# Kernel tuning notes

Measured on AMD Instinct MI355X. Metric: run time of the kernel, lower is better.

## Reference

```python
import jax, jax.numpy as jnp
import numpy as np

B, SQ, ST, SI = 8, 4096, 77, 16
C, DC, H = 1280, 2048, 20
DH = C // H  # 64
SCALE = 1.0 / np.sqrt(DH).astype(np.float32)
SCALE_ID = 1.0
SCALE_HAIR = 1.0


def setup_inputs() -> dict:
    key = jax.random.key(0)
    ks = jax.random.split(key, 12)
    std = 0.02
    return {
        "hidden_states": jax.random.normal(ks[0], (B, SQ, C), jnp.float32),
        "text_states": jax.random.normal(ks[1], (B, ST, DC), jnp.float32),
        "id_states": jax.random.normal(ks[2], (B, SI, DC), jnp.float32),
        "hair_states": jax.random.normal(ks[3], (B, SI, DC), jnp.float32),
        # weights stored as [in, out] (transpose of torch nn.Linear layout)
        "Wq": jax.random.normal(ks[4], (C, C), jnp.float32) * std,
        "Wk": jax.random.normal(ks[5], (DC, C), jnp.float32) * std,
        "Wv": jax.random.normal(ks[6], (DC, C), jnp.float32) * std,
        "Wo": jax.random.normal(ks[7], (C, C), jnp.float32) * std,
        "b_o": jnp.zeros((C,), jnp.float32),
        "Wk_id": jax.random.normal(ks[8], (DC, C), jnp.float32) * std,
        "Wv_id": jax.random.normal(ks[9], (DC, C), jnp.float32) * std,
        "Wk_hair": jax.random.normal(ks[10], (DC, C), jnp.float32) * std,
        "Wv_hair": jax.random.normal(ks[11], (DC, C), jnp.float32) * std,
    }


def _heads(x):
    # [B, S, C] -> [B, H, S, DH]
    b, s, _ = x.shape
    return x.reshape(b, s, H, DH).transpose(0, 2, 1, 3)


def _merge(x):
    # [B, H, S, DH] -> [B, S, C]
    b, h, s, d = x.shape
    return x.transpose(0, 2, 1, 3).reshape(b, s, h * d)


def _attend(q, k, v):
    # q: [B,H,Sq,DH], k/v: [B,H,Sk,DH]; fp32 scores (attn_fp32=True)
    scores = jnp.einsum("bhqd,bhkd->bhqk", q.astype(jnp.float32), k.astype(jnp.float32)) * SCALE
    p = jax.nn.softmax(scores, axis=-1)
    return jnp.einsum("bhqk,bhkd->bhqd", p, v.astype(jnp.float32))


def reference(hidden_states, text_states, id_states, hair_states, Wq, Wk, Wv, Wo, b_o, Wk_id, Wv_id, Wk_hair, Wv_hair):
    q = _heads(hidden_states @ Wq)
    # base cross-attention to text (standard diffusers AttnProcessor)
    base = _attend(q, _heads(text_states @ Wk), _heads(text_states @ Wv))
    result = _merge(base) @ Wo + b_o
    # ID branch: own K/V projections, shared query and to_out
    out_id = _attend(q, _heads(id_states @ Wk_id), _heads(id_states @ Wv_id))
    result = result + SCALE_ID * (_merge(out_id) @ Wo + b_o)
    # hair branch
    out_h = _attend(q, _heads(hair_states @ Wk_hair), _heads(hair_states @ Wv_hair))
    result = result + SCALE_HAIR * (_merge(out_h) @ Wo + b_o)
    return result
```

## Files before the change

### kernel.cpp

```cpp
#include <hip/hip_runtime.h>
#include <cstdint>
#include <cstddef>

typedef unsigned short u16;
typedef __attribute__((ext_vector_type(4))) float     f32x4_t;
typedef __attribute__((ext_vector_type(8))) __bf16    bf16x8_t;
typedef __attribute__((ext_vector_type(8))) u16       u16x8_t;
typedef __attribute__((ext_vector_type(4))) u16       u16x4_t;
typedef __attribute__((ext_vector_type(4))) float     fvec4_t;

#define DEVI __device__ __forceinline__

constexpr int Bn  = 8;
constexpr int SQn = 4096;
constexpr int STn = 77;
constexpr int SIn = 16;
constexpr int Cn  = 1280;
constexpr int DCn = 2048;
constexpr int Hn  = 20;
constexpr float SCALEf = 0.125f;
constexpr float L2E    = 1.4426950408889634f;

typedef const __attribute__((address_space(1))) void* gas_t;
typedef __attribute__((address_space(3))) void*       las_t;

DEVI u16 f2bf(float f) {
  union { float f; unsigned u; } cv; cv.f = f;
  unsigned u = cv.u;
  return (u16)((u + 0x7FFFu + ((u >> 16) & 1u)) >> 16);
}

__global__ __launch_bounds__(256) void cast_bf16_kernel(
    const float* __restrict__ src, u16* __restrict__ dst, int n8) {
  int i = blockIdx.x * 256 + threadIdx.x;
  if (i >= n8) return;
  const fvec4_t* s4 = (const fvec4_t*)src;
  fvec4_t a = s4[2 * i], b = s4[2 * i + 1];
  u16x8_t o;
  o[0] = f2bf(a[0]); o[1] = f2bf(a[1]); o[2] = f2bf(a[2]); o[3] = f2bf(a[3]);
  o[4] = f2bf(b[0]); o[5] = f2bf(b[1]); o[6] = f2bf(b[2]); o[7] = f2bf(b[3]);
  ((u16x8_t*)dst)[i] = o;
}

struct TrArgs {
  const float* src[8];
  u16*         dst[8];
  int          Kd[8];
};

__global__ __launch_bounds__(256) void transpose_cast_kernel(TrArgs ta) {
  int z = blockIdx.z;
  int K = ta.Kd[z];
  int k0 = blockIdx.x * 32;
  if (k0 >= K) return;
  int n0 = blockIdx.y * 32;
  __shared__ float tile[32][33];
  int tx = threadIdx.x & 31, ty = threadIdx.x >> 5;
  const float* src = ta.src[z];
#pragma unroll
  for (int i = 0; i < 4; i++) {
    int r = ty + 8 * i;
    tile[r][tx] = src[(size_t)(k0 + r) * Cn + n0 + tx];
  }
  __syncthreads();
  u16* dst = ta.dst[z];
#pragma unroll
  for (int i = 0; i < 4; i++) {
    int r = ty + 8 * i;
    dst[(size_t)(n0 + r) * K + k0 + tx] = f2bf(tile[tx][r]);
  }
}

template <int OUT_MODE, int A_HM>
__global__ __launch_bounds__(512, 2) void gemm256_kernel(
    const u16* __restrict__ A, const u16* __restrict__ Bt,
    void* __restrict__ Cout, const float* __restrict__ bias, int M, int K) {
  __shared__ __align__(16) u16 lds[(OUT_MODE == 2) ? 73728 : 65536];
  const int t = threadIdx.x;
  const int w = t >> 6, l = t & 63;
  const int wr = w >> 2, wc = w & 3;
  const int lr = l & 15;
  const int m0 = blockIdx.x * 256, n0 = blockIdx.y * 256;
  const int NT = K >> 6;

  auto bufp = [&](int cb, int op) -> u16* { return lds + (size_t)(cb * 2 + op) * 16384; };

  f32x4_t acc[8][4];
#pragma unroll
  for (int am = 0; am < 8; am++)
#pragma unroll
    for (int an = 0; an < 4; an++) {
      f32x4_t z = {0.f, 0.f, 0.f, 0.f};
      acc[am][an] = z;
    }

  auto stageAll = [&](int cb, int kt) {
    const int k0 = kt * 64;
#pragma unroll
    for (int i = 0; i < 4; i++) {
      int row = i * 64 + w * 8 + (l >> 3);
      int col16 = (l & 7) ^ (row & 7);
      const u16* ga;
      if (A_HM) {
        int gr = m0 + row, bb = gr >> 12, ss = gr & 4095;
        ga = A + (((size_t)bb * Hn + kt) * SQn + ss) * 64 + col16 * 8;
      } else {
        ga = A + (size_t)(m0 + row) * K + k0 + col16 * 8;
      }
      __builtin_amdgcn_global_load_lds((gas_t)ga, (las_t)(bufp(cb, 0) + (size_t)(i * 512 + w * 64) * 8), 16, 0, 0);
      const u16* gb = Bt + (size_t)(n0 + row) * K + k0 + col16 * 8;
      __builtin_amdgcn_global_load_lds((gas_t)gb, (las_t)(bufp(cb, 1) + (size_t)(i * 512 + w * 64) * 8), 16, 0, 0);
    }
  };
  auto readA8 = [&](bf16x8_t (&dst)[8], const u16* bA, int kh) {
#pragma unroll
    for (int m = 0; m < 8; m++) {
      int row = wr * 128 + m * 16 + lr;
      int slot = kh * 4 + (l >> 4);
      dst[m] = *(const bf16x8_t*)&bA[row * 64 + ((slot ^ (row & 7)) * 8)];
    }
  };
  auto readB4 = [&](bf16x8_t (&dst)[4], const u16* bB, int kh) {
#pragma unroll
    for (int n = 0; n < 4; n++) {
      int row = wc * 64 + n * 16 + lr;
      int slot = kh * 4 + (l >> 4);
      dst[n] = *(const bf16x8_t*)&bB[row * 64 + ((slot ^ (row & 7)) * 8)];
    }
  };
  auto mfma32 = [&](bf16x8_t (&Af)[8], bf16x8_t (&Bf)[4]) {
    __builtin_amdgcn_s_setprio(1);
#pragma unroll
    for (int m = 0; m < 8; m++)
#pragma unroll
      for (int n = 0; n < 4; n++)
        acc[m][n] = __builtin_amdgcn_mfma_f32_16x16x32_bf16(Af[m], Bf[n], acc[m][n], 0, 0, 0);
    __builtin_amdgcn_s_setprio(0);
  };

  stageAll(0, 0);
  stageAll(1, 1);
  asm volatile("s_waitcnt vmcnt(8)" ::: "memory");
  __builtin_amdgcn_sched_barrier(0);
  __builtin_amdgcn_s_barrier();

  bf16x8_t Af0[8], Bf0[4], Af1[8], Bf1[4];
  readA8(Af0, bufp(0, 0), 0);
  readB4(Bf0, bufp(0, 1), 0);
  asm volatile("s_waitcnt lgkmcnt(0)" ::: "memory");
  __builtin_amdgcn_sched_barrier(0);

  for (int kt = 0; kt < NT; kt++) {
    const int cb = kt & 1;
    const bool st = (kt + 2 < NT);

    readA8(Af1, bufp(cb, 0), 1);
    readB4(Bf1, bufp(cb, 1), 1);
    __builtin_amdgcn_sched_barrier(0);
    __builtin_amdgcn_s_barrier();
    if (st) stageAll(cb, kt + 2);
    mfma32(Af0, Bf0);
    asm volatile("s_waitcnt lgkmcnt(0)" ::: "memory");
    __builtin_amdgcn_sched_barrier(0);

    if (st) {
      asm volatile("s_waitcnt vmcnt(8)" ::: "memory");
    } else if (kt + 1 < NT) {
      asm volatile("s_waitcnt vmcnt(0)" ::: "memory");
    }
    __builtin_amdgcn_sched_barrier(0);
    __builtin_amdgcn_s_barrier();

    if (kt + 1 < NT) {
      readA8(Af0, bufp(cb ^ 1, 0), 0);
      readB4(Bf0, bufp(cb ^ 1, 1), 0);
      __builtin_amdgcn_sched_barrier(0);
    }
    mfma32(Af1, Bf1);
    asm volatile("s_waitcnt lgkmcnt(0)" ::: "memory");
    __builtin_amdgcn_sched_barrier(0);
  }

  if (OUT_MODE == 1) {
#pragma unroll
    for (int am = 0; am < 8; am++) {
      int rbase = m0 + wr * 128 + am * 16 + (l >> 4) * 4;
#pragma unroll
      for (int an = 0; an < 4; an++) {
        int col = n0 + wc * 64 + an * 16 + lr;
#pragma unroll
        for (int j = 0; j < 4; j++) {
          int r = rbase + j;
          ((float*)Cout)[(size_t)r * Cn + col] = acc[am][an][j] + 3.0f * bias[col];
        }
      }
    }
  } else {
    __syncthreads();
    u16* R = lds + (size_t)w * 9216;
#pragma unroll
    for (int am = 0; am < 8; am++)
#pragma unroll
      for (int an = 0; an < 4; an++)
#pragma unroll
        for (int j = 0; j < 4; j++) {
          int row = am * 16 + (l >> 4) * 4 + j;
          int g = an * 2 + (lr >> 3);
          int gp = g ^ (row & 7);
          R[row * 72 + gp * 8 + (lr & 7)] = f2bf(acc[am][an][j]);
        }
    const int hh = (n0 >> 6) + wc;
    const int rbase = m0 + wr * 128;
    const int bb = rbase >> 12;
    const int ssb = rbase & 4095;
    u16* dstW = (u16*)Cout + (((size_t)bb * Hn + hh) * SQn + ssb) * 64;
#pragma unroll
    for (int it = 0; it < 16; it++) {
      int rr = it * 8 + (l >> 3);
      int gr = l & 7;
      int gp = gr ^ (rr & 7);
      u16x8_t v = *(const u16x8_t*)&R[rr * 72 + gp * 8];
      *(u16x8_t*)&dstW[(size_t)rr * 64 + gr * 8] = v;
    }
  }
}

DEVI void gemm_body(const u16* __restrict__ A, const u16* __restrict__ Bt,
                    u16* __restrict__ Cout, int M, int S, int K, int mtile, int ntile) {
  __shared__ __align__(16) u16 lA[128 * 64];
  __shared__ __align__(16) u16 lB[128 * 64];
  const int t = threadIdx.x;
  const int w = t >> 6, l = t & 63;
  const int wr = w >> 1, wc = w & 1;
  const int m0 = mtile * 128, n0 = ntile * 128;
  const int lr = l & 15, lk = (l >> 4) * 8;

  f32x4_t acc[4][4];
#pragma unroll
  for (int m = 0; m < 4; m++)
#pragma unroll
    for (int n = 0; n < 4; n++) {
      f32x4_t z = {0.f, 0.f, 0.f, 0.f};
      acc[m][n] = z;
    }

  for (int k0 = 0; k0 < K; k0 += 64) {
    __syncthreads();
#pragma unroll
    for (int i = 0; i < 4; i++) {
      int c = i * 256 + t;
      int row = c >> 3, ch = c & 7;
      int rA = m0 + row;
      rA = rA < M ? rA : M - 1;
      const u16* ga = A + (size_t)rA * K + k0 + ch * 8;
      __builtin_amdgcn_global_load_lds((gas_t)ga, (las_t)&lA[(i * 256 + w * 64) * 8], 16, 0, 0);
      const u16* gb = Bt + (size_t)(n0 + row) * K + k0 + ch * 8;
      __builtin_amdgcn_global_load_lds((gas_t)gb, (las_t)&lB[(i * 256 + w * 64) * 8], 16, 0, 0);
    }
    __syncthreads();
#pragma unroll
    for (int kk = 0; kk < 2; kk++) {
      bf16x8_t af[4], bf[4];
#pragma unroll
      for (int m = 0; m < 4; m++)
        af[m] = *(const bf16x8_t*)&lA[(64 * wr + 16 * m + lr) * 64 + kk * 32 + lk];
#pragma unroll
      for (int n = 0; n < 4; n++)
        bf[n] = *(const bf16x8_t*)&lB[(64 * wc + 16 * n + lr) * 64 + kk * 32 + lk];
#pragma unroll
      for (int m = 0; m < 4; m++)
#pragma unroll
        for (int n = 0; n < 4; n++)
          acc[m][n] = __builtin_amdgcn_mfma_f32_16x16x32_bf16(af[m], bf[n], acc[m][n], 0, 0, 0);
    }
  }

  const int rj = (l >> 4) * 4;
  const int hh = ntile * 2 + wc;
#pragma unroll
  for (int m = 0; m < 4; m++) {
    int rbase = m0 + 64 * wr + 16 * m + rj;
#pragma unroll
    for (int n = 0; n < 4; n++) {
      int dd = 16 * n + lr;
#pragma unroll
      for (int j = 0; j < 4; j++) {
        int r = rbase + j;
        if (r < M) {
          int bb = r / S, ss = r - bb * S;
          Cout[(((size_t)bb * Hn + hh) * S + ss) * 64 + dd] = f2bf(acc[m][n][j]);
        }
      }
    }
  }
}

struct KV6 {
  const u16* A[6];
  const u16* Bt[6];
  u16*       Cp[6];
  int        M[6];
  int        S[6];
};

__global__ __launch_bounds__(256) void gemm_kv_kernel(KV6 kv) {
  int z = blockIdx.z;
  int M = kv.M[z];
  if ((int)blockIdx.x * 128 >= M) return;
  gemm_body(kv.A[z], kv.Bt[z], kv.Cp[z], M, kv.S[z], DCn, blockIdx.x, blockIdx.y);
}

__global__ __launch_bounds__(256) void attn_kernel(
    const u16* __restrict__ q,
    const u16* __restrict__ ktx, const u16* __restrict__ vtx,
    const u16* __restrict__ kid, const u16* __restrict__ vid,
    const u16* __restrict__ kh,  const u16* __restrict__ vh,
    u16* __restrict__ osum) {
  __shared__ __align__(16) u16 KP[4 * 16 * 136];
  __shared__ __align__(16) u16 Vt[64 * 128];

  const int t = threadIdx.x, w = t >> 6, l = t & 63;
  const int bh = blockIdx.y;
  const int lr = l & 15, lk = (l >> 4) * 8;

  const u16* qB   = q   + ((size_t)bh) * SQn * 64;
  const u16* ktxB = ktx + ((size_t)bh) * STn * 64;
  const u16* vtxB = vtx + ((size_t)bh) * STn * 64;
  const u16* kidB = kid + ((size_t)bh) * SIn * 64;
  const u16* vidB = vid + ((size_t)bh) * SIn * 64;
  const u16* khB  = kh  + ((size_t)bh) * SIn * 64;
  const u16* vhB  = vh  + ((size_t)bh) * SIn * 64;
  u16*       oB   = osum + ((size_t)bh) * SQn * 64;

  for (int i = t; i < 112 * 8; i += 256) {
    int row = i >> 3, ch = i & 7;
    u16x8_t vv;
#pragma unroll
    for (int x = 0; x < 8; x++) vv[x] = 0;
    if (row < 77)
      vv = *(const u16x8_t*)(ktxB + (size_t)row * 64 + ch * 8);
    else if (row >= 80 && row < 96)
      vv = *(const u16x8_t*)(kidB + (size_t)(row - 80) * 64 + ch * 8);
    else if (row >= 96)
      vv = *(const u16x8_t*)(khB + (size_t)(row - 96) * 64 + ch * 8);
    *(u16x8_t*)&KP[row * 72 + ch * 8] = vv;
  }
  for (int i = t; i < 128 * 8; i += 256) {
    int key = i >> 3, ch = i & 7;
    u16x8_t vv;
#pragma unroll
    for (int x = 0; x < 8; x++) vv[x] = 0;
    if (key < 77)
      vv = *(const u16x8_t*)(vtxB + (size_t)key * 64 + ch * 8);
    else if (key >= 80 && key < 96)
      vv = *(const u16x8_t*)(vidB + (size_t)(key - 80) * 64 + ch * 8);
    else if (key >= 96 && key < 112)
      vv = *(const u16x8_t*)(vhB + (size_t)(key - 96) * 64 + ch * 8);
    int G = key >> 3, wk = key & 7;
#pragma unroll
    for (int x = 0; x < 8; x++) {
      int d = ch * 8 + x;
      int Gs = G ^ x ^ ch;
      Vt[d * 128 + Gs * 8 + wk] = vv[x];
    }
  }
  __syncthreads();

  bf16x8_t kf[7][2];
#pragma unroll
  for (int tt = 0; tt < 7; tt++)
#pragma unroll
    for (int kk = 0; kk < 2; kk++)
      kf[tt][kk] = *(const bf16x8_t*)&KP[(tt * 16 + lr) * 72 + kk * 32 + lk];
  __syncthreads();

  u16* Pw = &KP[w * 16 * 136];
  {
    u16x4_t z4; z4[0] = 0; z4[1] = 0; z4[2] = 0; z4[3] = 0;
    *(u16x4_t*)&Pw[(l >> 2) * 136 + 112 + (l & 3) * 4] = z4;
  }

  for (int rt = 0; rt < 4; rt++) {
    const int s0 = blockIdx.x * 256 + w * 64 + rt * 16;
    bf16x8_t qf[2];
#pragma unroll
    for (int kk = 0; kk < 2; kk++)
      qf[kk] = *(const bf16x8_t*)&qB[(size_t)(s0 + lr) * 64 + kk * 32 + lk];

    f32x4_t sc[7];
#pragma unroll
    for (int tt = 0; tt < 7; tt++) {
      f32x4_t z = {0.f, 0.f, 0.f, 0.f};
      z = __builtin_amdgcn_mfma_f32_16x16x32_bf16(qf[0], kf[tt][0], z, 0, 0, 0);
      z = __builtin_amdgcn_mfma_f32_16x16x32_bf16(qf[1], kf[tt][1], z, 0, 0, 0);
      sc[tt] = z;
    }
#pragma unroll
    for (int tt = 0; tt < 7; tt++)
#pragma unroll
      for (int j = 0; j < 4; j++) sc[tt][j] *= SCALEf;
    if (lr >= 13) {
#pragma unroll
      for (int j = 0; j < 4; j++) sc[4][j] = -3.0e38f;
    }

    float mx[4], sm[4], inv[4];

#pragma unroll
    for (int j = 0; j < 4; j++) {
      float m = sc[0][j];
      m = fmaxf(m, sc[1][j]); m = fmaxf(m, sc[2][j]);
      m = fmaxf(m, sc[3][j]); m = fmaxf(m, sc[4][j]);
      mx[j] = m;
    }
#pragma unroll
    for (int d = 1; d < 16; d <<= 1)
#pragma unroll
      for (int j = 0; j < 4; j++) mx[j] = fmaxf(mx[j], __shfl_xor(mx[j], d));
#pragma unroll
    for (int j = 0; j < 4; j++) sm[j] = 0.f;
#pragma unroll
    for (int tt = 0; tt < 5; tt++)
#pragma unroll
      for (int j = 0; j < 4; j++) {
        float p = __builtin_amdgcn_exp2f((sc[tt][j] - mx[j]) * L2E);
        sc[tt][j] = p;
        sm[j] += p;
      }
#pragma unroll
    for (int d = 1; d < 16; d <<= 1)
#pragma unroll
      for (int j = 0; j < 4; j++) sm[j] += __shfl_xor(sm[j], d);
#pragma unroll
    for (int j = 0; j < 4; j++) inv[j] = __builtin_amdgcn_rcpf(sm[j]);
#pragma unroll
    for (int tt = 0; tt < 5; tt++)
#pragma unroll
      for (int j = 0; j < 4; j++) {
        __bf16 pb = (__bf16)(sc[tt][j] * inv[j]);
        Pw[((l >> 4) * 4 + j) * 136 + tt * 16 + lr] = *(u16*)&pb;
      }

#pragma unroll
    for (int j = 0; j < 4; j++) mx[j] = sc[5][j];
#pragma unroll
    for (int d = 1; d < 16; d <<= 1)
#pragma unroll
      for (int j = 0; j < 4; j++) mx[j] = fmaxf(mx[j], __shfl_xor(mx[j], d));
#pragma unroll
    for (int j = 0; j < 4; j++) {
      float p = __builtin_amdgcn_exp2f((sc[5][j] - mx[j]) * L2E);
      sc[5][j] = p;
      sm[j] = p;
    }
#pragma unroll
    for (int d = 1; d < 16; d <<= 1)
#pragma unroll
      for (int j = 0; j < 4; j++) sm[j] += __shfl_xor(sm[j], d);
#pragma unroll
    for (int j = 0; j < 4; j++) {
      __bf16 pb = (__bf16)(sc[5][j] * __builtin_amdgcn_rcpf(sm[j]));
      Pw[((l >> 4) * 4 + j) * 136 + 80 + lr] = *(u16*)&pb;
    }

#pragma unroll
    for (int j = 0; j < 4; j++) mx[j] = sc[6][j];
#pragma unroll
    for (int d = 1; d < 16; d <<= 1)
#pragma unroll
      for (int j = 0; j < 4; j++) mx[j] = fmaxf(mx[j], __shfl_xor(mx[j], d));
#pragma unroll
    for (int j = 0; j < 4; j++) {
      float p = __builtin_amdgcn_exp2f((sc[6][j] - mx[j]) * L2E);
      sc[6][j] = p;
      sm[j] = p;
    }
#pragma unroll
    for (int d = 1; d < 16; d <<= 1)
#pragma unroll
      for (int j = 0; j < 4; j++) sm[j] += __shfl_xor(sm[j], d);
#pragma unroll
    for (int j = 0; j < 4; j++) {
      __bf16 pb = (__bf16)(sc[6][j] * __builtin_amdgcn_rcpf(sm[j]));
      Pw[((l >> 4) * 4 + j) * 136 + 96 + lr] = *(u16*)&pb;
    }

    f32x4_t oacc[4];
#pragma unroll
    for (int n = 0; n < 4; n++) {
      f32x4_t z = {0.f, 0.f, 0.f, 0.f};
      oacc[n] = z;
    }
#pragma unroll
    for (int ktile = 0; ktile < 4; ktile++) {
      bf16x8_t pf = *(const bf16x8_t*)&Pw[lr * 136 + ktile * 32 + lk];
#pragma unroll
      for (int n = 0; n < 4; n++) {
        int d = 16 * n + lr;
        int Gs = (4 * ktile + (l >> 4)) ^ (d & 7) ^ ((d >> 3) & 7);
        bf16x8_t vf = *(const bf16x8_t*)&Vt[d * 128 + Gs * 8];
        oacc[n] = __builtin_amdgcn_mfma_f32_16x16x32_bf16(pf, vf, oacc[n], 0, 0, 0);
      }
    }
#pragma unroll
    for (int n = 0; n < 4; n++)
#pragma unroll
      for (int j = 0; j < 4; j++) {
        int srow = s0 + (l >> 4) * 4 + j;
        __bf16 ob = (__bf16)oacc[n][j];
        oB[(size_t)srow * 64 + 16 * n + lr] = *(u16*)&ob;
      }
  }
}

extern "C" void kernel_launch(void* const* d_in, const int* in_sizes, int n_in,
                              void* d_out, int out_size, void* d_ws, size_t ws_size,
                              hipStream_t stream) {
  (void)in_sizes; (void)n_in; (void)out_size; (void)ws_size;
  const float* hidden  = (const float*)d_in[0];
  const float* text    = (const float*)d_in[1];
  const float* ids     = (const float*)d_in[2];
  const float* hair    = (const float*)d_in[3];
  const float* Wq      = (const float*)d_in[4];
  const float* Wk      = (const float*)d_in[5];
  const float* Wv      = (const float*)d_in[6];
  const float* Wo      = (const float*)d_in[7];
  const float* b_o     = (const float*)d_in[8];
  const float* Wk_id   = (const float*)d_in[9];
  const float* Wv_id   = (const float*)d_in[10];
  const float* Wk_hair = (const float*)d_in[11];
  const float* Wv_hair = (const float*)d_in[12];
  float* out = (float*)d_out;

  char* ws = (char*)d_ws;
  size_t off = 0;
  auto carve = [&](size_t bytes) -> char* {
    char* p = ws + off;
    off += (bytes + 255) & ~(size_t)255;
    return p;
  };

  u16* h_bf    = (u16*)carve((size_t)Bn * SQn * Cn * 2);
  u16* q_bf    = (u16*)carve((size_t)Bn * SQn * Cn * 2);
  u16* text_bf = (u16*)carve((size_t)Bn * STn * DCn * 2);
  u16* id_bf   = (u16*)carve((size_t)Bn * SIn * DCn * 2);
  u16* hair_bf = (u16*)carve((size_t)Bn * SIn * DCn * 2);
  u16* Wq_t    = (u16*)carve((size_t)Cn * Cn * 2);
  u16* Wo_t    = (u16*)carve((size_t)Cn * Cn * 2);
  u16* Wk_t    = (u16*)carve((size_t)DCn * Cn * 2);
  u16* Wv_t    = (u16*)carve((size_t)DCn * Cn * 2);
  u16* Wkid_t  = (u16*)carve((size_t)DCn * Cn * 2);
  u16* Wvid_t  = (u16*)carve((size_t)DCn * Cn * 2);
  u16* Wkh_t   = (u16*)carve((size_t)DCn * Cn * 2);
  u16* Wvh_t   = (u16*)carve((size_t)DCn * Cn * 2);
  u16* k_text  = (u16*)carve((size_t)Bn * STn * Cn * 2);
  u16* v_text  = (u16*)carve((size_t)Bn * STn * Cn * 2);
  u16* k_id    = (u16*)carve((size_t)Bn * SIn * Cn * 2);
  u16* v_id    = (u16*)carve((size_t)Bn * SIn * Cn * 2);
  u16* k_hr    = (u16*)carve((size_t)Bn * SIn * Cn * 2);
  u16* v_hr    = (u16*)carve((size_t)Bn * SIn * Cn * 2);
  u16* attn_sum = h_bf;

  {
    int n8 = Bn * SQn * Cn / 8;
    cast_bf16_kernel<<<dim3((n8 + 255) / 256), 256, 0, stream>>>(hidden, h_bf, n8);
  }
  {
    int n8 = Bn * STn * DCn / 8;
    cast_bf16_kernel<<<dim3((n8 + 255) / 256), 256, 0, stream>>>(text, text_bf, n8);
  }
  {
    int n8 = Bn * SIn * DCn / 8;
    cast_bf16_kernel<<<dim3((n8 + 255) / 256), 256, 0, stream>>>(ids, id_bf, n8);
    cast_bf16_kernel<<<dim3((n8 + 255) / 256), 256, 0, stream>>>(hair, hair_bf, n8);
  }

  {
    TrArgs ta;
    ta.src[0] = Wq;      ta.dst[0] = Wq_t;   ta.Kd[0] = Cn;
    ta.src[1] = Wo;      ta.dst[1] = Wo_t;   ta.Kd[1] = Cn;
    ta.src[2] = Wk;      ta.dst[2] = Wk_t;   ta.Kd[2] = DCn;
    ta.src[3] = Wv;      ta.dst[3] = Wv_t;   ta.Kd[3] = DCn;
    ta.src[4] = Wk_id;   ta.dst[4] = Wkid_t; ta.Kd[4] = DCn;
    ta.src[5] = Wv_id;   ta.dst[5] = Wvid_t; ta.Kd[5] = DCn;
    ta.src[6] = Wk_hair; ta.dst[6] = Wkh_t;  ta.Kd[6] = DCn;
    ta.src[7] = Wv_hair; ta.dst[7] = Wvh_t;  ta.Kd[7] = DCn;
    transpose_cast_kernel<<<dim3(DCn / 32, Cn / 32, 8), 256, 0, stream>>>(ta);
  }

  gemm256_kernel<2, 0><<<dim3(Bn * SQn / 256, Cn / 256), 512, 0, stream>>>(
      h_bf, Wq_t, q_bf, nullptr, Bn * SQn, Cn);

  {
    KV6 kv;
    kv.A[0] = text_bf; kv.Bt[0] = Wk_t;   kv.Cp[0] = k_text; kv.M[0] = Bn * STn; kv.S[0] = STn;
    kv.A[1] = text_bf; kv.Bt[1] = Wv_t;   kv.Cp[1] = v_text; kv.M[1] = Bn * STn; kv.S[1] = STn;
    kv.A[2] = id_bf;   kv.Bt[2] = Wkid_t; kv.Cp[2] = k_id;   kv.M[2] = Bn * SIn; kv.S[2] = SIn;
    kv.A[3] = id_bf;   kv.Bt[3] = Wvid_t; kv.Cp[3] = v_id;   kv.M[3] = Bn * SIn; kv.S[3] = SIn;
    kv.A[4] = hair_bf; kv.Bt[4] = Wkh_t;  kv.Cp[4] = k_hr;   kv.M[4] = Bn * SIn; kv.S[4] = SIn;
    kv.A[5] = hair_bf; kv.Bt[5] = Wvh_t;  kv.Cp[5] = v_hr;   kv.M[5] = Bn * SIn; kv.S[5] = SIn;
    gemm_kv_kernel<<<dim3((Bn * STn + 127) / 128, Cn / 128, 6), 256, 0, stream>>>(kv);
  }

  attn_kernel<<<dim3(SQn / 256, Bn * Hn), 256, 0, stream>>>(
      q_bf, k_text, v_text, k_id, v_id, k_hr, v_hr, attn_sum);

  gemm256_kernel<1, 1><<<dim3(Bn * SQn / 256, Cn / 256), 512, 0, stream>>>(
      attn_sum, Wo_t, out, b_o, Bn * SQn, Cn);
}
```

Measured before the change: 480.8 us.

## Fuse fp32-to-bf16 cast of hidden states into the Q projection GEMM

Removes the standalone cast kernel for hidden_states and has a new Q GEMM kernel load fp32 A tiles into registers, convert to bf16, and write them swizzled into LDS, while B still uses direct global-to-LDS loads. This avoids writing and re-reading a 32768x1280 bf16 intermediate. The trade-off is that the GEMM now reads twice as many A bytes, each A tile is read by 5 column blocks, and the pipeline adds register staging and conversion work that could slow the main loop. The generic GEMM template is reduced to the fp32-output path.

```diff
diff --git a/kernel.cpp b/kernel.cpp
--- a/kernel.cpp
+++ b/kernel.cpp
@@ -71,11 +71,160 @@
   }
 }
 
+__global__ __launch_bounds__(512, 2) void gemm_q_fused_kernel(
+    const float* __restrict__ Af, const u16* __restrict__ Bt,
+    u16* __restrict__ Cout, int M, int K) {
+  __shared__ __align__(16) u16 lds[73728];
+  const int t = threadIdx.x;
+  const int w = t >> 6, l = t & 63;
+  const int wr = w >> 2, wc = w & 3;
+  const int lr = l & 15;
+  const int m0 = blockIdx.x * 256, n0 = blockIdx.y * 256;
+  const int NT = K >> 6;
+
+  auto bufp = [&](int cb, int op) -> u16* { return lds + (size_t)(cb * 2 + op) * 16384; };
+
+  f32x4_t acc[8][4];
+#pragma unroll
+  for (int am = 0; am < 8; am++)
+#pragma unroll
+    for (int an = 0; an < 4; an++) {
+      f32x4_t z = {0.f, 0.f, 0.f, 0.f};
+      acc[am][an] = z;
+    }
+
+  f32x4_t areg[8];
+  auto issueA = [&](int kt) {
+    const int k0 = kt * 64;
+#pragma unroll
+    for (int i = 0; i < 4; i++) {
+      int row = i * 64 + w * 8 + (l >> 3);
+      const float* ga = Af + (size_t)(m0 + row) * K + k0 + (l & 7) * 8;
+      areg[2 * i]     = *(const fvec4_t*)ga;
+      areg[2 * i + 1] = *(const fvec4_t*)(ga + 4);
+    }
+  };
+  auto writeA = [&](int cb) {
+#pragma unroll
+    for (int i = 0; i < 4; i++) {
+      int row = i * 64 + w * 8 + (l >> 3);
+      int gp = (l & 7) ^ (row & 7);
+      u16x8_t o;
+      o[0] = f2bf(areg[2 * i][0]);     o[1] = f2bf(areg[2 * i][1]);
+      o[2] = f2bf(areg[2 * i][2]);     o[3] = f2bf(areg[2 * i][3]);
+      o[4] = f2bf(areg[2 * i + 1][0]); o[5] = f2bf(areg[2 * i + 1][1]);
+      o[6] = f2bf(areg[2 * i + 1][2]); o[7] = f2bf(areg[2 * i + 1][3]);
+      *(u16x8_t*)&bufp(cb, 0)[row * 64 + gp * 8] = o;
+    }
+  };
+  auto issueB = [&](int cb, int kt) {
+    const int k0 = kt * 64;
+#pragma unroll
+    for (int i = 0; i < 4; i++) {
+      int row = i * 64 + w * 8 + (l >> 3);
+      int col16 = (l & 7) ^ (row & 7);
+      const u16* gb = Bt + (size_t)(n0 + row) * K + k0 + col16 * 8;
+      __builtin_amdgcn_global_load_lds((gas_t)gb, (las_t)(bufp(cb, 1) + (size_t)(i * 512 + w * 64) * 8), 16, 0, 0);
+    }
+  };
+  auto readA8 = [&](bf16x8_t (&dst)[8], const u16* bA, int kh) {
+#pragma unroll
+    for (int m = 0; m < 8; m++) {
+      int row = wr * 128 + m * 16 + lr;
+      int slot = kh * 4 + (l >> 4);
+      dst[m] = *(const bf16x8_t*)&bA[row * 64 + ((slot ^ (row & 7)) * 8)];
+    }
+  };
+  auto readB4 = [&](bf16x8_t (&dst)[4], const u16* bB, int kh) {
+#pragma unroll
+    for (int n = 0; n < 4; n++) {
+      int row = wc * 64 + n * 16 + lr;
+      int slot = kh * 4 + (l >> 4);
+      dst[n] = *(const bf16x8_t*)&bB[row * 64 + ((slot ^ (row & 7)) * 8)];
+    }
+  };
+  auto mfma32 = [&](bf16x8_t (&Afr)[8], bf16x8_t (&Bfr)[4]) {
+    __builtin_amdgcn_s_setprio(1);
+#pragma unroll
+    for (int m = 0; m < 8; m++)
+#pragma unroll
+      for (int n = 0; n < 4; n++)
+        acc[m][n] = __builtin_amdgcn_mfma_f32_16x16x32_bf16(Afr[m], Bfr[n], acc[m][n], 0, 0, 0);
+    __builtin_amdgcn_s_setprio(0);
+  };
+
+  issueA(0);
+  writeA(0);
+  issueA(1);
+  issueB(0, 0);
+  issueB(1, 1);
+  asm volatile("s_waitcnt vmcnt(4)" ::: "memory");
+  __builtin_amdgcn_sched_barrier(0);
+  writeA(1);
+  issueA(2);
+  asm volatile("s_waitcnt lgkmcnt(0)" ::: "memory");
+  __builtin_amdgcn_sched_barrier(0);
+  __builtin_amdgcn_s_barrier();
+
+  for (int kt = 0; kt < NT; kt++) {
+    const int cb = kt & 1;
+    const u16* bA = bufp(cb, 0);
+    const u16* bB = bufp(cb, 1);
+    bf16x8_t Afr[8], Bfr[4];
+
+    readA8(Afr, bA, 0);
+    readB4(Bfr, bB, 0);
+    asm volatile("s_waitcnt lgkmcnt(0)" ::: "memory");
+    __builtin_amdgcn_sched_barrier(0);
+    mfma32(Afr, Bfr);
+
+    readA8(Afr, bA, 1);
+    readB4(Bfr, bB, 1);
+    __builtin_amdgcn_s_barrier();
+    asm volatile("s_waitcnt vmcnt(0)" ::: "memory");
+    __builtin_amdgcn_sched_barrier(0);
+    if (kt + 2 < NT) writeA(cb);
+    if (kt + 3 < NT) issueA(kt + 3);
+    if (kt + 2 < NT) issueB(cb, kt + 2);
+    asm volatile("s_waitcnt lgkmcnt(0)" ::: "memory");
+    __builtin_amdgcn_sched_barrier(0);
+    mfma32(Afr, Bfr);
+    __builtin_amdgcn_s_barrier();
+  }
+
+  __syncthreads();
+  u16* R = lds + (size_t)w * 9216;
+#pragma unroll
+  for (int am = 0; am < 8; am++)
+#pragma unroll
+    for (int an = 0; an < 4; an++)
+#pragma unroll
+      for (int j = 0; j < 4; j++) {
+        int row = am * 16 + (l >> 4) * 4 + j;
+        int g = an * 2 + (lr >> 3);
+        int gp = g ^ (row & 7);
+        R[row * 72 + gp * 8 + (lr & 7)] = f2bf(acc[am][an][j]);
+      }
+  const int hh = (n0 >> 6) + wc;
+  const int rbase = m0 + wr * 128;
+  const int bb = rbase >> 12;
+  const int ssb = rbase & 4095;
+  u16* dstW = Cout + (((size_t)bb * Hn + hh) * SQn + ssb) * 64;
+#pragma unroll
+  for (int it = 0; it < 16; it++) {
+    int rr = it * 8 + (l >> 3);
+    int gr = l & 7;
+    int gp = gr ^ (rr & 7);
+    u16x8_t v = *(const u16x8_t*)&R[rr * 72 + gp * 8];
+    *(u16x8_t*)&dstW[(size_t)rr * 64 + gr * 8] = v;
+  }
+}
+
 template <int OUT_MODE, int A_HM>
 __global__ __launch_bounds__(512, 2) void gemm256_kernel(
     const u16* __restrict__ A, const u16* __restrict__ Bt,
     void* __restrict__ Cout, const float* __restrict__ bias, int M, int K) {
-  __shared__ __align__(16) u16 lds[(OUT_MODE == 2) ? 73728 : 65536];
+  __shared__ __align__(16) u16 lds[65536];
   const int t = threadIdx.x;
   const int w = t >> 6, l = t & 63;
   const int wr = w >> 2, wc = w & 3;
@@ -181,46 +330,17 @@
     __builtin_amdgcn_sched_barrier(0);
   }
 
-  if (OUT_MODE == 1) {
-#pragma unroll
-    for (int am = 0; am < 8; am++) {
-      int rbase = m0 + wr * 128 + am * 16 + (l >> 4) * 4;
-#pragma unroll
-      for (int an = 0; an < 4; an++) {
-        int col = n0 + wc * 64 + an * 16 + lr;
-#pragma unroll
-        for (int j = 0; j < 4; j++) {
-          int r = rbase + j;
-          ((float*)Cout)[(size_t)r * Cn + col] = acc[am][an][j] + 3.0f * bias[col];
-        }
+#pragma unroll
+  for (int am = 0; am < 8; am++) {
+    int rbase = m0 + wr * 128 + am * 16 + (l >> 4) * 4;
+#pragma unroll
+    for (int an = 0; an < 4; an++) {
+      int col = n0 + wc * 64 + an * 16 + lr;
+#pragma unroll
+      for (int j = 0; j < 4; j++) {
+        int r = rbase + j;
+        ((float*)Cout)[(size_t)r * Cn + col] = acc[am][an][j] + 3.0f * bias[col];
       }
-    }
-  } else {
-    __syncthreads();
-    u16* R = lds + (size_t)w * 9216;
-#pragma unroll
-    for (int am = 0; am < 8; am++)
-#pragma unroll
-      for (int an = 0; an < 4; an++)
-#pragma unroll
-        for (int j = 0; j < 4; j++) {
-          int row = am * 16 + (l >> 4) * 4 + j;
-          int g = an * 2 + (lr >> 3);
-          int gp = g ^ (row & 7);
-          R[row * 72 + gp * 8 + (lr & 7)] = f2bf(acc[am][an][j]);
-        }
-    const int hh = (n0 >> 6) + wc;
-    const int rbase = m0 + wr * 128;
-    const int bb = rbase >> 12;
-    const int ssb = rbase & 4095;
-    u16* dstW = (u16*)Cout + (((size_t)bb * Hn + hh) * SQn + ssb) * 64;
-#pragma unroll
-    for (int it = 0; it < 16; it++) {
-      int rr = it * 8 + (l >> 3);
-      int gr = l & 7;
-      int gp = gr ^ (rr & 7);
-      u16x8_t v = *(const u16x8_t*)&R[rr * 72 + gp * 8];
-      *(u16x8_t*)&dstW[(size_t)rr * 64 + gr * 8] = v;
     }
   }
 }
@@ -540,7 +660,7 @@
     return p;
   };
 
-  u16* h_bf    = (u16*)carve((size_t)Bn * SQn * Cn * 2);
+  u16* attn_sum = (u16*)carve((size_t)Bn * SQn * Cn * 2);
   u16* q_bf    = (u16*)carve((size_t)Bn * SQn * Cn * 2);
   u16* text_bf = (u16*)carve((size_t)Bn * STn * DCn * 2);
   u16* id_bf   = (u16*)carve((size_t)Bn * SIn * DCn * 2);
@@ -559,12 +679,7 @@
   u16* v_id    = (u16*)carve((size_t)Bn * SIn * Cn * 2);
   u16* k_hr    = (u16*)carve((size_t)Bn * SIn * Cn * 2);
   u16* v_hr    = (u16*)carve((size_t)Bn * SIn * Cn * 2);
-  u16* attn_sum = h_bf;
-
-  {
-    int n8 = Bn * SQn * Cn / 8;
-    cast_bf16_kernel<<<dim3((n8 + 255) / 256), 256, 0, stream>>>(hidden, h_bf, n8);
-  }
+
   {
     int n8 = Bn * STn * DCn / 8;
     cast_bf16_kernel<<<dim3((n8 + 255) / 256), 256, 0, stream>>>(text, text_bf, n8);
@@ -588,8 +703,8 @@
     transpose_cast_kernel<<<dim3(DCn / 32, Cn / 32, 8), 256, 0, stream>>>(ta);
   }
 
-  gemm256_kernel<2, 0><<<dim3(Bn * SQn / 256, Cn / 256), 512, 0, stream>>>(
-      h_bf, Wq_t, q_bf, nullptr, Bn * SQn, Cn);
+  gemm_q_fused_kernel<<<dim3(Bn * SQn / 256, Cn / 256), 512, 0, stream>>>(
+      hidden, Wq_t, q_bf, Bn * SQn, Cn);
 
   {
     KV6 kv;
```

After: 518.0 us. 7.7% more time.
